# Optimization experiments

Measured on AMD Instinct MI355X. Metric: run time of the kernel, lower is better.

## Reference

```python
import jax, jax.numpy as jnp
import numpy as np

B, T, V, E, L, H = 128, 512, 128, 64, 128, 512  # batch, seq, vocab, char_emb, latent, hidden


def setup_inputs() -> dict:
    key = jax.random.key(0)
    ks = jax.random.split(key, 12)
    r = lambda k, shape, s=0.05: jax.random.normal(k, shape, dtype=jnp.float32) * s
    return {
        "char_ids": jax.random.randint(ks[0], (B, T), 0, V),
        "z": jax.random.normal(ks[1], (B, L), dtype=jnp.float32),
        "emb": r(ks[2], (V, E)),
        "cw1": r(ks[3], (L, H)), "cb1": jnp.zeros((H,)), "cg1": jnp.ones((H,)), "cbeta1": jnp.zeros((H,)),
        "cw2": r(ks[4], (H, H)), "cb2": jnp.zeros((H,)), "cg2": jnp.ones((H,)), "cbeta2": jnp.zeros((H,)),
        "wih0": r(ks[5], (4 * H, E + H + 2)), "whh0": r(ks[6], (4 * H, H)),
        "bih0": jnp.zeros((4 * H,)), "bhh0": jnp.zeros((4 * H,)),
        "wih1": r(ks[7], (4 * H, H)), "whh1": r(ks[8], (4 * H, H)),
        "bih1": jnp.zeros((4 * H,)), "bhh1": jnp.zeros((4 * H,)),
        "wo1": r(ks[9], (H, H // 2)), "bo1": jnp.zeros((H // 2,)),
        "wo2": r(ks[10], (H // 2, 2)), "bo2": jnp.zeros((2,)),
        "init_timing": jnp.zeros((2,)),
    }


def _ln(x, g, b, eps=1e-5):
    m = jnp.mean(x, -1, keepdims=True)
    v = jnp.var(x, -1, keepdims=True)
    return (x - m) * jax.lax.rsqrt(v + eps) * g + b


def _lstm_cell(x, h, c, wih, whh, bih, bhh):
    # PyTorch gate order: i, f, g, o
    gates = x @ wih.T + bih + h @ whh.T + bhh
    i, f, g, o = jnp.split(gates, 4, axis=-1)
    c = jax.nn.sigmoid(f) * c + jax.nn.sigmoid(i) * jnp.tanh(g)
    h = jax.nn.sigmoid(o) * jnp.tanh(c)
    return h, c


def reference(char_ids, z, emb, cw1, cb1, cg1, cbeta1, cw2, cb2, cg2, cbeta2,
              wih0, whh0, bih0, bhh0, wih1, whh1, bih1, bhh1,
              wo1, bo1, wo2, bo2, init_timing):
    b = char_ids.shape[0]
    # condition encoder: Linear -> LN -> LeakyReLU(0.2), twice
    cond = jax.nn.leaky_relu(_ln(z @ cw1 + cb1, cg1, cbeta1), 0.2)
    cond = jax.nn.leaky_relu(_ln(cond @ cw2 + cb2, cg2, cbeta2), 0.2)  # (B, H)
    xs = jnp.transpose(emb[char_ids], (1, 0, 2))  # (T, B, E)
    h0 = jnp.zeros((b, H), jnp.float32)
    c0 = jnp.zeros((b, H), jnp.float32)
    h1 = jnp.zeros((b, H), jnp.float32)
    c1 = jnp.zeros((b, H), jnp.float32)
    prev = jnp.broadcast_to(init_timing, (b, 2))

    def step(carry, xt):
        h0, c0, h1, c1, prev = carry
        xin = jnp.concatenate([xt, cond, prev], axis=-1)  # (B, E+H+2)
        h0, c0 = _lstm_cell(xin, h0, c0, wih0, whh0, bih0, bhh0)
        h1, c1 = _lstm_cell(h0, h1, c1, wih1, whh1, bih1, bhh1)
        out = jax.nn.leaky_relu(h1 @ wo1 + bo1, 0.2) @ wo2 + bo2
        out = jax.nn.softplus(out) + 0.005  # (B, 2)
        return (h0, c0, h1, c1, out), out

    _, ys = jax.lax.scan(step, (h0, c0, h1, c1, prev), xs)
    return jnp.transpose(ys, (1, 0, 2))  # (B, T, 2)
```

## Files before the change

kernel.cpp:

```cpp
#include <hip/hip_runtime.h>

#define Bn 128
#define Tn 512
#define Vn 128
#define En 64
#define Ln 128
#define Hn 512
#define G4 2048
#define WGS 256
#define NTHR 512
#define NALL (WGS * NTHR)
#define LSTR 520
#define GRPS 8
#define WPG 32
#define RPG 16

typedef unsigned short u16;
typedef unsigned int u32;
typedef __bf16 bf16x8 __attribute__((ext_vector_type(8)));
typedef float f32x4 __attribute__((ext_vector_type(4)));
typedef u32 u32x4 __attribute__((ext_vector_type(4)));

__device__ inline float bf2f(u16 h) {
    u32 u = ((u32)h) << 16;
    float f;
    __builtin_memcpy(&f, &u, 4);
    return f;
}
__device__ inline u16 f2bf(float f) {
    u32 u;
    __builtin_memcpy(&u, &f, 4);
    u32 r = (u + 0x7fffu + ((u >> 16) & 1u)) >> 16;
    return (u16)r;
}
__device__ inline u32 f2u(float f) { u32 u; __builtin_memcpy(&u, &f, 4); return u; }
__device__ inline float u2f(u32 u) { float f; __builtin_memcpy(&f, &u, 4); return f; }
__device__ inline float sigm(float x) { return 1.f / (1.f + expf(-x)); }
__device__ inline float leaky(float x) { return x > 0.f ? x : 0.2f * x; }
__device__ inline float softplus(float x) {
    return x > 0.f ? x + log1pf(expf(-x)) : log1pf(expf(x));
}

__device__ inline void cload16(const u32* p, u32* w) {
    u32x4 v0, v1, v2, v3;
    asm volatile(
        "global_load_dwordx4 %0, %4, off sc0 sc1\n\t"
        "global_load_dwordx4 %1, %4, off offset:16 sc0 sc1\n\t"
        "global_load_dwordx4 %2, %4, off offset:32 sc0 sc1\n\t"
        "global_load_dwordx4 %3, %4, off offset:48 sc0 sc1\n\t"
        "s_waitcnt vmcnt(0)"
        : "=&v"(v0), "=&v"(v1), "=&v"(v2), "=&v"(v3)
        : "v"(p)
        : "memory");
    *(u32x4*)(w) = v0;
    *(u32x4*)(w + 4) = v1;
    *(u32x4*)(w + 8) = v2;
    *(u32x4*)(w + 12) = v3;
}
__device__ inline u32 cload1(const u32* p) {
    u32 v;
    asm volatile("global_load_dword %0, %1, off sc0 sc1\n\ts_waitcnt vmcnt(0)"
                 : "=v"(v) : "v"(p) : "memory");
    return v;
}
__device__ inline void cwait() { asm volatile("s_waitcnt vmcnt(0)" ::: "memory"); }
__device__ inline void cstore1(u32* p, u32 v) {
    asm volatile("global_store_dword %0, %1, off sc0 sc1" :: "v"(p), "v"(v) : "memory");
}

#define OFF_FLAGS  0x000000
#define OFF_B1SUM  0x002000
#define OFF_WP     0x004000
#define OFF_BIAS0  0x008000
#define OFF_CPAR   0x00A000
#define OFF_H0P    0x010000
#define OFF_H1P    0x050000
#define OFF_PART   0x090000
#define OFF_WO1TH  0x0B0000
#define OFF_WO1TL  0x0F0000
#define OFF_ZF     0x130000
#define OFF_CW1F   0x140000
#define OFF_CW2F   0x180000
#define OFF_CONDF  0x280000
#define OFF_YBUF   0x2C0000
#define OFF_BASE0  0x300000
#define OFF_EMBW   0x400000
#define OFF_W0HI   0x500000
#define OFF_W0LO   0x700000
#define OFF_W1HI   0x900000
#define OFF_W1LO   0xB00000
#define OFF_WI1HI  0xD00000
#define OFF_WI1LO  0xF00000

__device__ inline void gbar_heavy(int* cnt, int* gen) {
    __syncthreads();
    if (threadIdx.x == 0) {
        __threadfence();
        int g = __hip_atomic_load(gen, __ATOMIC_RELAXED, __HIP_MEMORY_SCOPE_AGENT);
        int arrived = __hip_atomic_fetch_add(cnt, 1, __ATOMIC_ACQ_REL, __HIP_MEMORY_SCOPE_AGENT);
        if (arrived == WGS - 1) {
            __hip_atomic_store(cnt, 0, __ATOMIC_RELAXED, __HIP_MEMORY_SCOPE_AGENT);
            __hip_atomic_store(gen, g + 1, __ATOMIC_RELEASE, __HIP_MEMORY_SCOPE_AGENT);
        } else {
            while (__hip_atomic_load(gen, __ATOMIC_ACQUIRE, __HIP_MEMORY_SCOPE_AGENT) == g)
                __builtin_amdgcn_s_sleep(1);
        }
        __threadfence();
    }
    __syncthreads();
}

__device__ inline void poll32(const u32* gf, u32 sq) {
    const int l = threadIdx.x & 31;
    for (;;) {
        u32 v = cload1(gf + l);
        if (__all((int)(v >= sq))) break;
        __builtin_amdgcn_s_sleep(2);
    }
}
__device__ inline void poll16(const u32* gf, u32 sq) {
    const int l = threadIdx.x & 15;
    for (;;) {
        u32 v = cload1(gf + l);
        if (__all((int)(v >= sq))) break;
        __builtin_amdgcn_s_sleep(2);
    }
}

__device__ inline void unpack16(const u32* w, u16* ph, u16* pl) {
    u32 hd[8], ld[8];
#pragma unroll
    for (int i = 0; i < 8; ++i) {
        hd[i] = (w[2 * i] & 0xFFFFu) | (w[2 * i + 1] << 16);
        ld[i] = (w[2 * i] >> 16) | (w[2 * i + 1] & 0xFFFF0000u);
    }
    *(u32x4*)(ph) = *(const u32x4*)(hd);
    *(u32x4*)(ph + 8) = *(const u32x4*)(hd + 4);
    *(u32x4*)(pl) = *(const u32x4*)(ld);
    *(u32x4*)(pl + 8) = *(const u32x4*)(ld + 4);
}

#define MF(a, b, c) __builtin_amdgcn_mfma_f32_16x16x32_bf16(a, b, c, 0, 0, 0)

__device__ inline f32x4 gemm16_3(const u16* __restrict__ Ah, const u16* __restrict__ Al,
                                 const u16* __restrict__ Bhb, const u16* __restrict__ Blb,
                                 int colb, int n, int q) {
    const u16* Bh = Bhb + (size_t)(colb + n) * Hn;
    const u16* Bl = Blb + (size_t)(colb + n) * Hn;
    const int a0 = n * LSTR;
    f32x4 c0 = {0.f, 0.f, 0.f, 0.f}, c1 = c0, c2 = c0;
#pragma unroll 4
    for (int it = 0; it < 16; ++it) {
        const int ko = it * 32 + q * 8;
        bf16x8 bh = *(const bf16x8*)(Bh + ko);
        bf16x8 bl = *(const bf16x8*)(Bl + ko);
        bf16x8 ah = *(const bf16x8*)(Ah + a0 + ko);
        bf16x8 al = *(const bf16x8*)(Al + a0 + ko);
        c0 = MF(ah, bh, c0);
        c1 = MF(al, bh, c1);
        c2 = MF(ah, bl, c2);
    }
    return c0 + c1 + c2;
}

__device__ inline f32x4 gemm16_s2(const u16* __restrict__ Ah, const u16* __restrict__ Al,
                                  const u16* __restrict__ Bhb, int colb, int n, int q) {
    const u16* Bh = Bhb + (size_t)(colb + n) * Hn;
    const int a0 = n * LSTR;
    f32x4 c0 = {0.f, 0.f, 0.f, 0.f}, c1 = c0;
#pragma unroll 4
    for (int it = 0; it < 16; ++it) {
        const int ko = it * 32 + q * 8;
        bf16x8 bh = *(const bf16x8*)(Bh + ko);
        bf16x8 ah = *(const bf16x8*)(Ah + a0 + ko);
        bf16x8 al = *(const bf16x8*)(Al + a0 + ko);
        c0 = MF(ah, bh, c0);
        c1 = MF(al, bh, c1);
    }
    return c0 + c1;
}

__device__ inline f32x4 gemm16_regB3(const u16* __restrict__ Ah, const u16* __restrict__ Al,
                                     const bf16x8* wa, const bf16x8* wb, int n, int q) {
    const int a0 = n * LSTR;
    f32x4 c0 = {0.f, 0.f, 0.f, 0.f}, c1 = c0, c2 = c0;
#pragma unroll
    for (int it = 0; it < 16; ++it) {
        const int ko = it * 32 + q * 8;
        bf16x8 ah = *(const bf16x8*)(Ah + a0 + ko);
        bf16x8 al = *(const bf16x8*)(Al + a0 + ko);
        c0 = MF(ah, wa[it], c0);
        c1 = MF(al, wa[it], c1);
        c2 = MF(ah, wb[it], c2);
    }
    return c0 + c1 + c2;
}

__device__ inline f32x4 gemm16_regB2(const u16* __restrict__ Ah, const u16* __restrict__ Al,
                                     const bf16x8* wb, int n, int q) {
    const int a0 = n * LSTR;
    f32x4 c0 = {0.f, 0.f, 0.f, 0.f}, c1 = c0;
#pragma unroll
    for (int it = 0; it < 16; ++it) {
        const int ko = it * 32 + q * 8;
        bf16x8 ah = *(const bf16x8*)(Ah + a0 + ko);
        bf16x8 al = *(const bf16x8*)(Al + a0 + ko);
        c0 = MF(ah, wb[it], c0);
        c1 = MF(al, wb[it], c1);
    }
    return c0 + c1;
}

__device__ inline f32x4 gemm16_ldsB3(const u16* __restrict__ Ah, const u16* __restrict__ Al,
                                     const u16* __restrict__ Bh, const u16* __restrict__ Bl,
                                     int n, int q) {
    const int a0 = n * LSTR;
    f32x4 c0 = {0.f, 0.f, 0.f, 0.f}, c1 = c0, c2 = c0;
#pragma unroll 4
    for (int it = 0; it < 16; ++it) {
        const int ko = it * 32 + q * 8;
        bf16x8 bh = *(const bf16x8*)(Bh + a0 + ko);
        bf16x8 bl = *(const bf16x8*)(Bl + a0 + ko);
        bf16x8 ah = *(const bf16x8*)(Ah + a0 + ko);
        bf16x8 al = *(const bf16x8*)(Al + a0 + ko);
        c0 = MF(ah, bh, c0);
        c1 = MF(al, bh, c1);
        c2 = MF(ah, bl, c2);
    }
    return c0 + c1 + c2;
}

__device__ inline void stage(float* dst, const void* src, int n, int gtid, bool isbf) {
    if (isbf) {
        const u16* s = (const u16*)src;
        for (int e = gtid; e < n; e += NALL) dst[e] = bf2f(s[e]);
    } else {
        const float* s = (const float*)src;
        for (int e = gtid; e < n; e += NALL) dst[e] = s[e];
    }
}
__device__ inline void stage_split(u16* hi, u16* lo, const void* src, int n, int gtid, bool isbf) {
    if (isbf) {
        const u16* s = (const u16*)src;
        for (int e = gtid; e < n; e += NALL) { hi[e] = s[e]; lo[e] = 0; }
    } else {
        const float* s = (const float*)src;
        for (int e = gtid; e < n; e += NALL) {
            float w = s[e];
            u16 h = f2bf(w);
            hi[e] = h;
            lo[e] = f2bf(w - bf2f(h));
        }
    }
}

template <bool ISBF>
__device__ inline float ldw(const void* p, size_t i) {
    if constexpr (ISBF) return bf2f(((const u16*)p)[i]);
    else return ((const float*)p)[i];
}

template <bool ISBF>
__device__ void phase5(const void* wih0, const void* emb, const float* __restrict__ condf,
                       const float* __restrict__ bias0f, float* __restrict__ base0,
                       float* __restrict__ embW, int gtid) {
    const int cc = gtid & 2047;
    const int bb0 = gtid >> 11;
    float b = bias0f[cc];
    float a0 = b, a1 = b, a2 = b, a3 = b;
    const float* c0p = condf + (size_t)bb0 * Hn;
    const float* c1p = condf + (size_t)(bb0 + 32) * Hn;
    const float* c2p = condf + (size_t)(bb0 + 64) * Hn;
    const float* c3p = condf + (size_t)(bb0 + 96) * Hn;
    const size_t wb = (size_t)cc * 578 + 64;
    for (int k = 0; k < Hn; ++k) {
        float w = ldw<ISBF>(wih0, wb + k);
        a0 += c0p[k] * w; a1 += c1p[k] * w; a2 += c2p[k] * w; a3 += c3p[k] * w;
    }
    base0[(size_t)bb0 * G4 + cc] = a0;
    base0[(size_t)(bb0 + 32) * G4 + cc] = a1;
    base0[(size_t)(bb0 + 64) * G4 + cc] = a2;
    base0[(size_t)(bb0 + 96) * G4 + cc] = a3;
    float e0 = 0.f, e1 = 0.f, e2 = 0.f, e3 = 0.f;
    const size_t wb2 = (size_t)cc * 578;
    for (int k = 0; k < En; ++k) {
        float w = ldw<ISBF>(wih0, wb2 + k);
        e0 += ldw<ISBF>(emb, (size_t)bb0 * En + k) * w;
        e1 += ldw<ISBF>(emb, (size_t)(bb0 + 32) * En + k) * w;
        e2 += ldw<ISBF>(emb, (size_t)(bb0 + 64) * En + k) * w;
        e3 += ldw<ISBF>(emb, (size_t)(bb0 + 96) * En + k) * w;
    }
    embW[(size_t)bb0 * G4 + cc] = e0;
    embW[(size_t)(bb0 + 32) * G4 + cc] = e1;
    embW[(size_t)(bb0 + 64) * G4 + cc] = e2;
    embW[(size_t)(bb0 + 96) * G4 + cc] = e3;
}

__device__ inline void ln_leaky_row(const float* __restrict__ x, const float* __restrict__ gamma,
                                    const float* __restrict__ beta, float* __restrict__ out,
                                    float* red) {
    int tid = threadIdx.x;
    float v = x[tid];
    float s = v, s2 = v * v;
    for (int off = 32; off; off >>= 1) {
        s += __shfl_down(s, off);
        s2 += __shfl_down(s2, off);
    }
    int wv = tid >> 6;
    if ((tid & 63) == 0) { red[wv * 2] = s; red[wv * 2 + 1] = s2; }
    __syncthreads();
    if (tid == 0) {
        float ts = 0.f, ts2 = 0.f;
        for (int i = 0; i < 8; ++i) { ts += red[i * 2]; ts2 += red[i * 2 + 1]; }
        float m = ts / 512.f;
        float var = ts2 / 512.f - m * m;
        red[16] = m;
        red[17] = rsqrtf(var + 1e-5f);
    }
    __syncthreads();
    float m = red[16], rs = red[17];
    out[tid] = leaky((v - m) * rs * gamma[tid] + beta[tid]);
    __syncthreads();
}

__global__ void init_flags_kernel(int* flags) { flags[threadIdx.x] = 0; }

__global__ __launch_bounds__(NTHR, 2) void gen_kernel(
    const int* __restrict__ char_ids, const void* z, const void* emb,
    const void* cw1, const void* cb1, const void* cg1, const void* cbeta1,
    const void* cw2, const void* cb2, const void* cg2, const void* cbeta2,
    const void* wih0, const void* whh0, const void* bih0, const void* bhh0,
    const void* wih1, const void* whh1, const void* bih1, const void* bhh1,
    const void* wo1, const void* bo1, const void* wo2, const void* bo2,
    const void* init_t, void* outp, char* __restrict__ ws) {
    __shared__ u16 lh0h[RPG * LSTR];
    __shared__ u16 lh0l[RPG * LSTR];
    __shared__ u16 lh1h[RPG * LSTR];
    __shared__ u16 lh1l[RPG * LSTR];
    __shared__ u16 lwoh[16 * LSTR];
    __shared__ u16 lwol[16 * LSTR];
    __shared__ float smemx[1024];
    __shared__ float pvs[32];
    __shared__ float red[34];

    int* flags = (int*)(ws + OFF_FLAGS);
    float* b1sum = (float*)(ws + OFF_B1SUM);
    float* wpb = (float*)(ws + OFF_WP);
    float* bias0f = (float*)(ws + OFF_BIAS0);
    float* cpar = (float*)(ws + OFF_CPAR);
    u32* h0p = (u32*)(ws + OFF_H0P);
    u32* h1p = (u32*)(ws + OFF_H1P);
    float* partf = (float*)(ws + OFF_PART);
    u16* wo1Th = (u16*)(ws + OFF_WO1TH);
    u16* wo1Tl = (u16*)(ws + OFF_WO1TL);
    float* zf = (float*)(ws + OFF_ZF);
    float* cw1f = (float*)(ws + OFF_CW1F);
    float* cw2f = (float*)(ws + OFF_CW2F);
    float* condf = (float*)(ws + OFF_CONDF);
    float* ybuf = (float*)(ws + OFF_YBUF);
    float* base0 = (float*)(ws + OFF_BASE0);
    float* embW = (float*)(ws + OFF_EMBW);
    u16* W0hi = (u16*)(ws + OFF_W0HI);
    u16* W0lo = (u16*)(ws + OFF_W0LO);
    u16* W1hi = (u16*)(ws + OFF_W1HI);
    u16* W1lo = (u16*)(ws + OFF_W1LO);
    u16* Wi1hi = (u16*)(ws + OFF_WI1HI);
    u16* Wi1lo = (u16*)(ws + OFF_WI1LO);
    float* wo1f = base0;

    const bool isbf = (((const u32*)cg1)[0] == 0x3F803F80u);

    const int g = blockIdx.x;
    const int tid = threadIdx.x;
    const int wv = tid >> 6;
    const int grp = g >> 5;
    const int ut = g & 31;
    const int mat = wv >> 2;
    const int gw = wv & 3;
    const int R0g = grp * RPG;
    const int colb = gw * 512 + ut * 16;
    const int lane = tid & 63;
    const int n = lane & 15;
    const int q = lane >> 4;
    const int gtid = g * NTHR + tid;
    const f32x4 Z4 = {0.f, 0.f, 0.f, 0.f};

    u32* gf = (u32*)flags + grp * 64;
    u32* gf2 = (u32*)flags + grp * 64 + 32;
    u32* gfl = gf + ut;
    int* hcnt = flags + 512;
    int* hgen = flags + 528;
    float* part = partf + grp * 1024;

    stage_split(W0hi, W0lo, whh0, G4 * Hn, gtid, isbf);
    stage_split(W1hi, W1lo, whh1, G4 * Hn, gtid, isbf);
    stage_split(Wi1hi, Wi1lo, wih1, G4 * Hn, gtid, isbf);
    stage(zf, z, Bn * Ln, gtid, isbf);
    stage(cw1f, cw1, Ln * Hn, gtid, isbf);
    stage(cw2f, cw2, Hn * Hn, gtid, isbf);
    stage(cpar + 0, cg1, 512, gtid, isbf);
    stage(cpar + 512, cbeta1, 512, gtid, isbf);
    stage(cpar + 1024, cg2, 512, gtid, isbf);
    stage(cpar + 1536, cbeta2, 512, gtid, isbf);
    stage(cpar + 2048, bo1, 256, gtid, isbf);
    stage(cpar + 2304, bo2, 2, gtid, isbf);
    stage(cpar + 2560, cb2, 512, gtid, isbf);
    stage(cpar + 3072, cb1, 512, gtid, isbf);
    stage(cpar + 3584, wo2, 256 * 2, gtid, isbf);
    stage(wo1f, wo1, Hn * 256, gtid, isbf);
    if (gtid < Bn * Hn) { cstore1(h0p + gtid, 0); cstore1(h1p + gtid, 0); }
    if (isbf) {
        if (gtid < G4) b1sum[gtid] = bf2f(((const u16*)bih1)[gtid]) + bf2f(((const u16*)bhh1)[gtid]);
        if (gtid < G4) bias0f[gtid] = bf2f(((const u16*)bih0)[gtid]) + bf2f(((const u16*)bhh0)[gtid]);
        if (gtid < 4096) {
            size_t ix = (size_t)(gtid >> 1) * 578 + 576 + (gtid & 1);
            wpb[gtid] = bf2f(((const u16*)wih0)[ix]);
        }
    } else {
        if (gtid < G4) b1sum[gtid] = ((const float*)bih1)[gtid] + ((const float*)bhh1)[gtid];
        if (gtid < G4) bias0f[gtid] = ((const float*)bih0)[gtid] + ((const float*)bhh0)[gtid];
        if (gtid < 4096) {
            size_t ix = (size_t)(gtid >> 1) * 578 + 576 + (gtid & 1);
            wpb[gtid] = ((const float*)wih0)[ix];
        }
    }
    gbar_heavy(hcnt, hgen);
    if (gtid < Bn * Hn) {
        int bb = gtid >> 9, nn = gtid & 511;
        float a = cpar[3072 + nn];
        const float* zr = zf + bb * Ln;
        for (int k = 0; k < Ln; ++k) a += zr[k] * cw1f[k * Hn + nn];
        ybuf[gtid] = a;
    }
    for (int e = gtid; e < 256 * Hn; e += NALL) {
        int nn = e >> 9, kk = e & 511;
        float w = wo1f[kk * 256 + nn];
        u16 hv = f2bf(w);
        wo1Th[e] = hv;
        wo1Tl[e] = f2bf(w - bf2f(hv));
    }
    gbar_heavy(hcnt, hgen);
    if (g < Bn) ln_leaky_row(ybuf + g * Hn, cpar + 0, cpar + 512, condf + g * Hn, red);
    gbar_heavy(hcnt, hgen);
    if (g < Bn) {
        float a = cpar[2560 + tid];
        const float* crow = condf + g * Hn;
        for (int k = 0; k < Hn; ++k) a += crow[k] * cw2f[k * Hn + tid];
        ybuf[g * Hn + tid] = a;
    }
    gbar_heavy(hcnt, hgen);
    if (g < Bn) ln_leaky_row(ybuf + g * Hn, cpar + 1024, cpar + 1536, condf + g * Hn, red);
    gbar_heavy(hcnt, hgen);
    if (gtid < Bn * Hn) {
        if (isbf) phase5<true>(wih0, emb, condf, bias0f, base0, embW, gtid);
        else phase5<false>(wih0, emb, condf, bias0f, base0, embW, gtid);
    }
    gbar_heavy(hcnt, hgen);

    const bool headwg = (ut < 16);
    bf16x8 wA[16], wB[16];
    {
        const u16* BhA = (mat == 0 ? W0hi : W1hi) + (size_t)(colb + n) * Hn;
        const u16* BhB;
        if (isbf) {
            if (mat == 1) BhB = Wi1hi + (size_t)(colb + n) * Hn;
            else if (headwg && wv == 0) BhB = wo1Th + (size_t)(ut * 16 + n) * Hn;
            else BhB = BhA;
        } else {
            BhB = (mat == 0 ? W0lo : W1lo) + (size_t)(colb + n) * Hn;
        }
#pragma unroll
        for (int it = 0; it < 16; ++it) {
            wA[it] = *(const bf16x8*)(BhA + it * 32 + q * 8);
            wB[it] = *(const bf16x8*)(BhB + it * 32 + q * 8);
        }
    }
    if (!isbf && headwg) {
        for (int e = tid; e < 16 * Hn; e += NTHR) {
            int col = e >> 9, k = e & 511;
            lwoh[col * LSTR + k] = wo1Th[(size_t)(ut * 16 + col) * Hn + k];
            lwol[col * LSTR + k] = wo1Tl[(size_t)(ut * 16 + col) * Hn + k];
        }
    }

    float c0 = 0.f, c1 = 0.f;
    const int lr = tid >> 4;
    const int un = tid & 15;
    const int bb = R0g + lr;
    const int uu = ut * 16 + un;
    const float* bo1f = cpar + 2048;
    const float* bo2f = cpar + 2304;
    const float* wo2f = cpar + 3584;
    const int srow = tid >> 5;
    const int blk = tid & 31;
    const int kub = blk * 16;
    f32x4 acc1c = Z4;

    for (int e = tid; e < RPG * LSTR; e += NTHR) {
        lh0h[e] = 0; lh0l[e] = 0; lh1h[e] = 0; lh1l[e] = 0;
    }
    if (tid < 32) pvs[tid] = isbf ? bf2f(((const u16*)init_t)[tid & 1])
                                  : ((const float*)init_t)[tid & 1];

    float b0v[4], wpv[8], b1v[4];
    if (tid < 256) {
#pragma unroll
        for (int gi = 0; gi < 4; ++gi) {
            int cc = gi * 512 + uu;
            b0v[gi] = base0[(size_t)bb * G4 + cc];
            wpv[2 * gi] = wpb[2 * cc];
            wpv[2 * gi + 1] = wpb[2 * cc + 1];
            b1v[gi] = b1sum[cc];
        }
    }
    __syncthreads();

    for (int t = 0; t < Tn; ++t) {
        if (mat == 0) {
            f32x4 a = isbf ? gemm16_regB2(lh0h, lh0l, wA, n, q)
                           : gemm16_regB3(lh0h, lh0l, wA, wB, n, q);
#pragma unroll
            for (int r = 0; r < 4; ++r)
                smemx[gw * 256 + (q * 4 + r) * 16 + n] = a[r];
        }
        float ew0, ew1, ew2, ew3;
        if (tid < 256) {
            int id = char_ids[bb * Tn + t];
            const float* er = embW + (size_t)id * G4 + uu;
            ew0 = er[0]; ew1 = er[512]; ew2 = er[1024]; ew3 = er[1536];
        }
        if (t >= 1) {
            if (wv == 7) poll32(gf, 2 * (u32)t);
            __syncthreads();
            if (blk != ut) {
                u32 w[16];
                cload16(h1p + (size_t)(R0g + srow) * Hn + kub, w);
                unpack16(w, lh1h + srow * LSTR + kub, lh1l + srow * LSTR + kub);
            }
        }
        __syncthreads();
        if (headwg && wv == 0 && t >= 1) {
            f32x4 ha = isbf ? gemm16_regB2(lh1h, lh1l, wB, n, q)
                            : gemm16_ldsB3(lh1h, lh1l, lwoh, lwol, n, q);
            float p[4][2];
#pragma unroll
            for (int r = 0; r < 4; ++r) {
                float hv = leaky(ha[r] + bo1f[ut * 16 + n]);
                p[r][0] = hv * wo2f[(ut * 16 + n) * 2];
                p[r][1] = hv * wo2f[(ut * 16 + n) * 2 + 1];
            }
#pragma unroll
            for (int r = 0; r < 4; ++r)
#pragma unroll
                for (int j = 0; j < 2; ++j) {
                    float s = p[r][j];
                    s += __shfl_xor(s, 1, 16);
                    s += __shfl_xor(s, 2, 16);
                    s += __shfl_xor(s, 4, 16);
                    s += __shfl_xor(s, 8, 16);
                    p[r][j] = s;
                }
            if (n == 0) {
#pragma unroll
                for (int r = 0; r < 4; ++r)
#pragma unroll
                    for (int j = 0; j < 2; ++j) {
                        int row = q * 4 + r;
                        cstore1((u32*)(part + (row * 2 + j) * 16 + ut), f2u(p[r][j]));
                    }
            }
            cwait();
            if (tid == 0) cstore1(gf2 + ut, (u32)t);
        }
        if (mat == 1) {
            acc1c = isbf ? gemm16_regB2(lh1h, lh1l, wA, n, q)
                         : gemm16_regB3(lh1h, lh1l, wA, wB, n, q);
        }
        if (t >= 1 && wv == 4) {
            poll16(gf2, (u32)t);
            if (lane < 32) {
                int l = tid - 256;
                int row = l >> 1, j = l & 1;
                u32 hw[16];
                cload16((const u32*)(part + (row * 2 + j) * 16), hw);
                float s = bo2f[j];
#pragma unroll
                for (int i = 0; i < 16; ++i) s += u2f(hw[i]);
                float y = softplus(s) + 0.005f;
                pvs[row * 2 + j] = y;
                if (ut == 0) {
                    size_t oi = ((size_t)(R0g + row) * Tn + (t - 1)) * 2 + j;
                    if (isbf) ((u16*)outp)[oi] = f2bf(y);
                    else ((float*)outp)[oi] = y;
                }
            }
        }
        __syncthreads();
        if (tid < 256) {
            float pv0 = pvs[lr * 2], pv1 = pvs[lr * 2 + 1];
            float gv[4];
            gv[0] = smemx[0 * 256 + lr * 16 + un] + b0v[0] + ew0 + pv0 * wpv[0] + pv1 * wpv[1];
            gv[1] = smemx[1 * 256 + lr * 16 + un] + b0v[1] + ew1 + pv0 * wpv[2] + pv1 * wpv[3];
            gv[2] = smemx[2 * 256 + lr * 16 + un] + b0v[2] + ew2 + pv0 * wpv[4] + pv1 * wpv[5];
            gv[3] = smemx[3 * 256 + lr * 16 + un] + b0v[3] + ew3 + pv0 * wpv[6] + pv1 * wpv[7];
            float ig = sigm(gv[0]), fg = sigm(gv[1]), gg = tanhf(gv[2]), og = sigm(gv[3]);
            c0 = fg * c0 + ig * gg;
            float h = og * tanhf(c0);
            u16 hv = f2bf(h);
            u16 lv = f2bf(h - bf2f(hv));
            lh0h[lr * LSTR + uu] = hv;
            lh0l[lr * LSTR + uu] = lv;
            cstore1(h0p + (size_t)bb * Hn + uu, (u32)hv | ((u32)lv << 16));
        }
        cwait();
        __syncthreads();
        if (tid == 0) cstore1(gfl, 2 * (u32)t + 1);

        if (wv == 0) poll32(gf, 2 * (u32)t + 1);
        __syncthreads();
        if (blk != ut) {
            u32 w[16];
            cload16(h0p + (size_t)(R0g + srow) * Hn + kub, w);
            unpack16(w, lh0h + srow * LSTR + kub, lh0l + srow * LSTR + kub);
        }
        __syncthreads();
        if (mat == 1) {
            f32x4 a = isbf ? gemm16_s2(lh0h, lh0l, Wi1hi, colb, n, q)
                           : gemm16_3(lh0h, lh0l, Wi1hi, Wi1lo, colb, n, q);
            acc1c = acc1c + a;
#pragma unroll
            for (int r = 0; r < 4; ++r)
                smemx[gw * 256 + (q * 4 + r) * 16 + n] = acc1c[r];
        }
        __syncthreads();
        if (tid < 256) {
            float gv[4];
#pragma unroll
            for (int gi = 0; gi < 4; ++gi)
                gv[gi] = smemx[gi * 256 + lr * 16 + un] + b1v[gi];
            float ig = sigm(gv[0]), fg = sigm(gv[1]), gg = tanhf(gv[2]), og = sigm(gv[3]);
            c1 = fg * c1 + ig * gg;
            float h = og * tanhf(c1);
            u16 hv = f2bf(h);
            u16 lv = f2bf(h - bf2f(hv));
            lh1h[lr * LSTR + uu] = hv;
            lh1l[lr * LSTR + uu] = lv;
            cstore1(h1p + (size_t)bb * Hn + uu, (u32)hv | ((u32)lv << 16));
        }
        cwait();
        __syncthreads();
        if (tid == 0) cstore1(gfl, 2 * (u32)t + 2);
    }

    if (wv == 0) poll32(gf, 2 * (u32)Tn);
    __syncthreads();
    if (blk != ut) {
        u32 w[16];
        cload16(h1p + (size_t)(R0g + srow) * Hn + kub, w);
        unpack16(w, lh1h + srow * LSTR + kub, lh1l + srow * LSTR + kub);
    }
    __syncthreads();
    if (headwg && wv == 0) {
        f32x4 ha = isbf ? gemm16_regB2(lh1h, lh1l, wB, n, q)
                        : gemm16_ldsB3(lh1h, lh1l, lwoh, lwol, n, q);
        float p[4][2];
#pragma unroll
        for (int r = 0; r < 4; ++r) {
            float hv = leaky(ha[r] + bo1f[ut * 16 + n]);
            p[r][0] = hv * wo2f[(ut * 16 + n) * 2];
            p[r][1] = hv * wo2f[(ut * 16 + n) * 2 + 1];
        }
#pragma unroll
        for (int r = 0; r < 4; ++r)
#pragma unroll
            for (int j = 0; j < 2; ++j) {
                float s = p[r][j];
                s += __shfl_xor(s, 1, 16);
                s += __shfl_xor(s, 2, 16);
                s += __shfl_xor(s, 4, 16);
                s += __shfl_xor(s, 8, 16);
                p[r][j] = s;
            }
        if (n == 0) {
#pragma unroll
            for (int r = 0; r < 4; ++r)
#pragma unroll
                for (int j = 0; j < 2; ++j) {
                    int row = q * 4 + r;
                    cstore1((u32*)(part + (row * 2 + j) * 16 + ut), f2u(p[r][j]));
                }
        }
        cwait();
        if (tid == 0) cstore1(gf2 + ut, (u32)Tn);
    }
    if (ut == 0 && wv == 0) {
        poll16(gf2, (u32)Tn);
        if (tid < 32) {
            int row = tid >> 1, j = tid & 1;
            u32 hw[16];
            cload16((const u32*)(part + (row * 2 + j) * 16), hw);
            float s = bo2f[j];
#pragma unroll
            for (int i = 0; i < 16; ++i) s += u2f(hw[i]);
            float y = softplus(s) + 0.005f;
            size_t oi = ((size_t)(R0g + row) * Tn + (Tn - 1)) * 2 + j;
            if (isbf) ((u16*)outp)[oi] = f2bf(y);
            else ((float*)outp)[oi] = y;
        }
    }
}

extern "C" void kernel_launch(void* const* d_in, const int* in_sizes, int n_in,
                              void* d_out, int out_size, void* d_ws, size_t ws_size,
                              hipStream_t stream) {
    (void)in_sizes; (void)n_in; (void)out_size; (void)ws_size;
    init_flags_kernel<<<1, 1024, 0, stream>>>((int*)d_ws);
    gen_kernel<<<WGS, NTHR, 0, stream>>>(
        (const int*)d_in[0], d_in[1], d_in[2], d_in[3], d_in[4], d_in[5], d_in[6], d_in[7],
        d_in[8], d_in[9], d_in[10], d_in[11], d_in[12], d_in[13], d_in[14], d_in[15], d_in[16],
        d_in[17], d_in[18], d_in[19], d_in[20], d_in[21], d_in[22], d_in[23],
        d_out, (char*)d_ws);
}
```

Before: 8.653 ms.

## Compute output head redundantly per workgroup to drop cross-WG head synchronization

For bf16 inputs, each workgroup now computes the full output MLP head for its 16 rows locally. All 8 waves each handle 32 of the 256 head columns, with weights held in registers, and the partial sums are reduced through shared memory. This removes the global partial-sum buffer and the poll on per-WG head flags each timestep, a global synchronization on the serial critical path. In exchange every workgroup does 16x redundant head GEMM work and holds more registers for the extra weight fragments. The fp32 path keeps the old scheme.

```diff
diff --git a/kernel.cpp b/kernel.cpp
--- a/kernel.cpp
+++ b/kernel.cpp
@@ -230,6 +230,38 @@
     return c0 + c1 + c2;
 }
 
+#define FOR16(X) X(0) X(1) X(2) X(3) X(4) X(5) X(6) X(7) X(8) X(9) X(10) X(11) X(12) X(13) X(14) X(15)
+#define DECLH(i) bf16x8 wHa##i, wHb##i;
+#define LOADH(i) \
+    wHa##i = *(const bf16x8*)(hbase + (i) * 32 + q * 8); \
+    wHb##i = *(const bf16x8*)(hbase + 16 * Hn + (i) * 32 + q * 8);
+#define HGEMM(i) { \
+    bf16x8 ah_ = *(const bf16x8*)(lh1h + a0h + (i) * 32 + q * 8); \
+    bf16x8 al_ = *(const bf16x8*)(lh1l + a0h + (i) * 32 + q * 8); \
+    cA0 = MF(ah_, wHa##i, cA0); cA1 = MF(al_, wHa##i, cA1); \
+    cB0 = MF(ah_, wHb##i, cB0); cB1 = MF(al_, wHb##i, cB1); }
+#define REDHEAD() { \
+    const int a0h = n * LSTR; \
+    f32x4 cA0 = Z4, cA1 = Z4, cB0 = Z4, cB1 = Z4; \
+    FOR16(HGEMM) \
+    f32x4 hAx = cA0 + cA1, hBx = cB0 + cB1; \
+    float hp[4][2]; \
+    _Pragma("unroll") for (int r = 0; r < 4; ++r) { \
+        float hva = leaky(hAx[r] + bo1f[hc0]); \
+        float hvb = leaky(hBx[r] + bo1f[hc1]); \
+        hp[r][0] = hva * wo2f[hc0 * 2] + hvb * wo2f[hc1 * 2]; \
+        hp[r][1] = hva * wo2f[hc0 * 2 + 1] + hvb * wo2f[hc1 * 2 + 1]; } \
+    _Pragma("unroll") for (int r = 0; r < 4; ++r) \
+        _Pragma("unroll") for (int j = 0; j < 2; ++j) { \
+            float s_ = hp[r][j]; \
+            s_ += __shfl_xor(s_, 1, 16); s_ += __shfl_xor(s_, 2, 16); \
+            s_ += __shfl_xor(s_, 4, 16); s_ += __shfl_xor(s_, 8, 16); \
+            hp[r][j] = s_; } \
+    if (n == 0) { \
+        _Pragma("unroll") for (int r = 0; r < 4; ++r) { \
+            hpart[wv * 32 + (q * 4 + r) * 2 + 0] = hp[r][0]; \
+            hpart[wv * 32 + (q * 4 + r) * 2 + 1] = hp[r][1]; } } }
+
 __device__ inline void stage(float* dst, const void* src, int n, int gtid, bool isbf) {
     if (isbf) {
         const u16* s = (const u16*)src;
@@ -340,6 +372,7 @@
     __shared__ u16 lwoh[16 * LSTR];
     __shared__ u16 lwol[16 * LSTR];
     __shared__ float smemx[1024];
+    __shared__ float hpart[256];
     __shared__ float pvs[32];
     __shared__ float red[34];
 
@@ -459,20 +492,18 @@
 
     const bool headwg = (ut < 16);
     bf16x8 wA[16], wB[16];
+    FOR16(DECLH)
     {
         const u16* BhA = (mat == 0 ? W0hi : W1hi) + (size_t)(colb + n) * Hn;
-        const u16* BhB;
+#pragma unroll
+        for (int it = 0; it < 16; ++it) wA[it] = *(const bf16x8*)(BhA + it * 32 + q * 8);
         if (isbf) {
-            if (mat == 1) BhB = Wi1hi + (size_t)(colb + n) * Hn;
-            else if (headwg && wv == 0) BhB = wo1Th + (size_t)(ut * 16 + n) * Hn;
-            else BhB = BhA;
+            const u16* hbase = wo1Th + (size_t)(wv * 32 + n) * Hn;
+            FOR16(LOADH)
         } else {
-            BhB = (mat == 0 ? W0lo : W1lo) + (size_t)(colb + n) * Hn;
-        }
-#pragma unroll
-        for (int it = 0; it < 16; ++it) {
-            wA[it] = *(const bf16x8*)(BhA + it * 32 + q * 8);
-            wB[it] = *(const bf16x8*)(BhB + it * 32 + q * 8);
+            const u16* BhB = (mat == 0 ? W0lo : W1lo) + (size_t)(colb + n) * Hn;
+#pragma unroll
+            for (int it = 0; it < 16; ++it) wB[it] = *(const bf16x8*)(BhB + it * 32 + q * 8);
         }
     }
     if (!isbf && headwg) {
@@ -494,6 +525,8 @@
     const int srow = tid >> 5;
     const int blk = tid & 31;
     const int kub = blk * 16;
+    const int hc0 = wv * 32 + n;
+    const int hc1 = hc0 + 16;
     f32x4 acc1c = Z4;
 
     for (int e = tid; e < RPG * LSTR; e += NTHR) {
@@ -539,9 +572,10 @@
             }
         }
         __syncthreads();
-        if (headwg && wv == 0 && t >= 1) {
-            f32x4 ha = isbf ? gemm16_regB2(lh1h, lh1l, wB, n, q)
-                            : gemm16_ldsB3(lh1h, lh1l, lwoh, lwol, n, q);
+        if (isbf) {
+            if (t >= 1) REDHEAD();
+        } else if (headwg && wv == 0 && t >= 1) {
+            f32x4 ha = gemm16_ldsB3(lh1h, lh1l, lwoh, lwol, n, q);
             float p[4][2];
 #pragma unroll
             for (int r = 0; r < 4; ++r) {
@@ -576,7 +610,7 @@
             acc1c = isbf ? gemm16_regB2(lh1h, lh1l, wA, n, q)
                          : gemm16_regB3(lh1h, lh1l, wA, wB, n, q);
         }
-        if (t >= 1 && wv == 4) {
+        if (!isbf && t >= 1 && wv == 4) {
             poll16(gf2, (u32)t);
             if (lane < 32) {
                 int l = tid - 256;
@@ -590,12 +624,26 @@
                 pvs[row * 2 + j] = y;
                 if (ut == 0) {
                     size_t oi = ((size_t)(R0g + row) * Tn + (t - 1)) * 2 + j;
-                    if (isbf) ((u16*)outp)[oi] = f2bf(y);
-                    else ((float*)outp)[oi] = y;
+                    ((float*)outp)[oi] = y;
                 }
             }
         }
         __syncthreads();
+        if (isbf) {
+            if (t >= 1 && tid < 32) {
+                int row = tid >> 1, j = tid & 1;
+                float s = bo2f[j];
+#pragma unroll
+                for (int w8 = 0; w8 < 8; ++w8) s += hpart[w8 * 32 + row * 2 + j];
+                float y = softplus(s) + 0.005f;
+                pvs[row * 2 + j] = y;
+                if (ut == 0) {
+                    size_t oi = ((size_t)(R0g + row) * Tn + (t - 1)) * 2 + j;
+                    ((u16*)outp)[oi] = f2bf(y);
+                }
+            }
+            __syncthreads();
+        }
         if (tid < 256) {
             float pv0 = pvs[lr * 2], pv1 = pvs[lr * 2 + 1];
             float gv[4];
@@ -652,60 +700,82 @@
         if (tid == 0) cstore1(gfl, 2 * (u32)t + 2);
     }
 
-    if (wv == 0) poll32(gf, 2 * (u32)Tn);
-    __syncthreads();
-    if (blk != ut) {
-        u32 w[16];
-        cload16(h1p + (size_t)(R0g + srow) * Hn + kub, w);
-        unpack16(w, lh1h + srow * LSTR + kub, lh1l + srow * LSTR + kub);
-    }
-    __syncthreads();
-    if (headwg && wv == 0) {
-        f32x4 ha = isbf ? gemm16_regB2(lh1h, lh1l, wB, n, q)
-                        : gemm16_ldsB3(lh1h, lh1l, lwoh, lwol, n, q);
-        float p[4][2];
-#pragma unroll
-        for (int r = 0; r < 4; ++r) {
-            float hv = leaky(ha[r] + bo1f[ut * 16 + n]);
-            p[r][0] = hv * wo2f[(ut * 16 + n) * 2];
-            p[r][1] = hv * wo2f[(ut * 16 + n) * 2 + 1];
-        }
-#pragma unroll
-        for (int r = 0; r < 4; ++r)
-#pragma unroll
-            for (int j = 0; j < 2; ++j) {
-                float s = p[r][j];
-                s += __shfl_xor(s, 1, 16);
-                s += __shfl_xor(s, 2, 16);
-                s += __shfl_xor(s, 4, 16);
-                s += __shfl_xor(s, 8, 16);
-                p[r][j] = s;
-            }
-        if (n == 0) {
+    if (isbf) {
+        if (ut == 0) {
+            if (wv == 0) poll32(gf, 2 * (u32)Tn);
+            __syncthreads();
+            if (blk != ut) {
+                u32 w[16];
+                cload16(h1p + (size_t)(R0g + srow) * Hn + kub, w);
+                unpack16(w, lh1h + srow * LSTR + kub, lh1l + srow * LSTR + kub);
+            }
+            __syncthreads();
+            REDHEAD();
+            __syncthreads();
+            if (tid < 32) {
+                int row = tid >> 1, j = tid & 1;
+                float s = bo2f[j];
+#pragma unroll
+                for (int w8 = 0; w8 < 8; ++w8) s += hpart[w8 * 32 + row * 2 + j];
+                float y = softplus(s) + 0.005f;
+                size_t oi = ((size_t)(R0g + row) * Tn + (Tn - 1)) * 2 + j;
+                ((u16*)outp)[oi] = f2bf(y);
+            }
+        }
+    } else {
+        if (wv == 0) poll32(gf, 2 * (u32)Tn);
+        __syncthreads();
+        if (blk != ut) {
+            u32 w[16];
+            cload16(h1p + (size_t)(R0g + srow) * Hn + kub, w);
+            unpack16(w, lh1h + srow * LSTR + kub, lh1l + srow * LSTR + kub);
+        }
+        __syncthreads();
+        if (headwg && wv == 0) {
+            f32x4 ha = gemm16_ldsB3(lh1h, lh1l, lwoh, lwol, n, q);
+            float p[4][2];
+#pragma unroll
+            for (int r = 0; r < 4; ++r) {
+                float hv = leaky(ha[r] + bo1f[ut * 16 + n]);
+                p[r][0] = hv * wo2f[(ut * 16 + n) * 2];
+                p[r][1] = hv * wo2f[(ut * 16 + n) * 2 + 1];
+            }
 #pragma unroll
             for (int r = 0; r < 4; ++r)
 #pragma unroll
                 for (int j = 0; j < 2; ++j) {
-                    int row = q * 4 + r;
-                    cstore1((u32*)(part + (row * 2 + j) * 16 + ut), f2u(p[r][j]));
+                    float s = p[r][j];
+                    s += __shfl_xor(s, 1, 16);
+                    s += __shfl_xor(s, 2, 16);
+                    s += __shfl_xor(s, 4, 16);
+                    s += __shfl_xor(s, 8, 16);
+                    p[r][j] = s;
                 }
-        }
-        cwait();
-        if (tid == 0) cstore1(gf2 + ut, (u32)Tn);
-    }
-    if (ut == 0 && wv == 0) {
-        poll16(gf2, (u32)Tn);
-        if (tid < 32) {
-            int row = tid >> 1, j = tid & 1;
-            u32 hw[16];
-            cload16((const u32*)(part + (row * 2 + j) * 16), hw);
-            float s = bo2f[j];
-#pragma unroll
-            for (int i = 0; i < 16; ++i) s += u2f(hw[i]);
-            float y = softplus(s) + 0.005f;
-            size_t oi = ((size_t)(R0g + row) * Tn + (Tn - 1)) * 2 + j;
-            if (isbf) ((u16*)outp)[oi] = f2bf(y);
-            else ((float*)outp)[oi] = y;
+            if (n == 0) {
+#pragma unroll
+                for (int r = 0; r < 4; ++r)
+#pragma unroll
+                    for (int j = 0; j < 2; ++j) {
+                        int row = q * 4 + r;
+                        cstore1((u32*)(part + (row * 2 + j) * 16 + ut), f2u(p[r][j]));
+                    }
+            }
+            cwait();
+            if (tid == 0) cstore1(gf2 + ut, (u32)Tn);
+        }
+        if (ut == 0 && wv == 0) {
+            poll16(gf2, (u32)Tn);
+            if (tid < 32) {
+                int row = tid >> 1, j = tid & 1;
+                u32 hw[16];
+                cload16((const u32*)(part + (row * 2 + j) * 16), hw);
+                float s = bo2f[j];
+#pragma unroll
+                for (int i = 0; i < 16; ++i) s += u2f(hw[i]);
+                float y = softplus(s) + 0.005f;
+                size_t oi = ((size_t)(R0g + row) * Tn + (Tn - 1)) * 2 + j;
+                ((float*)outp)[oi] = y;
+            }
         }
     }
 }
```

Result: slower. 13.18 ms (+52.4%).
